# Kernel tuning notes

Hardware: AMD Instinct MI355X
Metric: run time of the kernel (lower is better)

## Reference

```python
import jax, jax.numpy as jnp
import numpy as np

B, H, S, D = 2, 12, 4096, 64

def setup_inputs() -> dict:
    key = jax.random.key(0)
    kq, kk, kv = jax.random.split(key, 3)
    Q = jax.random.normal(kq, (B, H, S, D), dtype=jnp.float32)
    K = jax.random.normal(kk, (B, H, S, D), dtype=jnp.float32)
    V = jax.random.normal(kv, (B, H, S, D), dtype=jnp.float32)
    attn_mask = jnp.zeros((1, 1, 1, 1), dtype=bool)  # unused by the original forward
    return {"Q": Q, "K": K, "V": V, "attn_mask": attn_mask}

def reference(Q, K, V, attn_mask):
    d_k = K.shape[3]
    # scores: [B, H, S, S] -- naive full materialization, matching the original
    scores = jnp.einsum("bhqd,bhkd->bhqk", Q, K) / np.sqrt(d_k).astype(Q.dtype)
    attn = jax.nn.softmax(scores, axis=-1)
    context = jnp.einsum("bhqk,bhkd->bhqd", attn, V)
    return context
```

## Files before the change

### kernel.cpp

```cpp
#include <hip/hip_runtime.h>

typedef _Float16 half4_t __attribute__((ext_vector_type(4)));
typedef _Float16 half8_t __attribute__((ext_vector_type(8)));
typedef __fp16  fp16x2_t __attribute__((ext_vector_type(2)));
typedef float floatx4 __attribute__((ext_vector_type(4)));

constexpr int S_  = 4096;
constexpr int D_  = 64;
constexpr int NBH = 24;
constexpr int BM  = 128;
constexpr int BN  = 64;
constexpr float SC2 = 0.125f * 1.44269504088896340736f;

__global__ __launch_bounds__(256) void preconv(
    const float* __restrict__ K, const float* __restrict__ V,
    _Float16* __restrict__ Kh, _Float16* __restrict__ Vh)
{
  __shared__ float tile[64 * 68];
  const int kt = blockIdx.x, bh = blockIdx.y, tid = threadIdx.x;
  const size_t tbase = ((size_t)bh * 64 + kt) * 4096;
#pragma unroll
  for (int it = 0; it < 2; ++it) {
    size_t i = tbase + (size_t)(tid + 256 * it) * 8;
    float4 a = *(const float4*)(K + i);
    float4 b = *(const float4*)(K + i + 4);
    *(half8_t*)(Kh + i) = (half8_t){
      (_Float16)(a.x*SC2),(_Float16)(a.y*SC2),(_Float16)(a.z*SC2),(_Float16)(a.w*SC2),
      (_Float16)(b.x*SC2),(_Float16)(b.y*SC2),(_Float16)(b.z*SC2),(_Float16)(b.w*SC2) };
  }
#pragma unroll
  for (int it = 0; it < 4; ++it) {
    int r  = (tid >> 4) + 16 * it;
    int c4 = (tid & 15) * 4;
    *(float4*)(&tile[r * 68 + c4]) = *(const float4*)(V + tbase + (size_t)r * 64 + c4);
  }
  __syncthreads();
  const int d = tid >> 2;
  _Float16 out[16];
#pragma unroll
  for (int j = 0; j < 16; ++j) {
    int key = 32 * (j >> 3) + 16 * ((j >> 2) & 1) + 4 * (tid & 3) + (j & 3);
    out[j] = (_Float16)tile[key * 68 + d];
  }
  _Float16* dst = Vh + tbase + (size_t)d * 64 + (tid & 3) * 16;
  *(half8_t*)(dst)     = *(half8_t*)(&out[0]);
  *(half8_t*)(dst + 8) = *(half8_t*)(&out[8]);
}


__device__ __forceinline__ void async16(const _Float16* g, _Float16* l) {
  __builtin_amdgcn_global_load_lds((const __attribute__((address_space(1))) void*)g,
                                   (__attribute__((address_space(3))) void*)l, 16, 0, 0);
}

__global__ __launch_bounds__(512, 4) void fattn2(
    const float* __restrict__ Qf, const _Float16* __restrict__ Kh,
    const _Float16* __restrict__ Vh, float* __restrict__ O)
{
  __shared__ __align__(16) _Float16 smem[6 * 4096];

  const int tid  = threadIdx.x;
  const int lane = tid & 63;
  const int w    = tid >> 6;
  const int g    = lane >> 4;
  const int m    = lane & 15;
  const int qh   = w & 3;
  const int kh2  = w >> 2;

  const int bid  = blockIdx.x;
  const int xcd  = bid & 7;
  const int slot = bid >> 3;
  const int bh   = xcd * 3 + (slot >> 5);
  const int qblk = slot & 31;
  const size_t base = (size_t)bh * S_ * D_;
  const int q0g = qblk * BM + qh * 32;

  half8_t qf[2][2];
#pragma unroll
  for (int qt = 0; qt < 2; ++qt)
#pragma unroll
    for (int ks = 0; ks < 2; ++ks) {
      const float4* qp = (const float4*)(Qf + base + (size_t)(q0g + qt*16 + m) * D_ + 8*g + 32*ks);
      float4 a = qp[0], b = qp[1];
      qf[qt][ks] = (half8_t){ (_Float16)a.x,(_Float16)a.y,(_Float16)a.z,(_Float16)a.w,
                              (_Float16)b.x,(_Float16)b.y,(_Float16)b.z,(_Float16)b.w };
    }

  floatx4 oacc[2][4];
#pragma unroll
  for (int qt = 0; qt < 2; ++qt)
#pragma unroll
    for (int db = 0; db < 4; ++db) oacc[qt][db] = (floatx4){0.f,0.f,0.f,0.f};
  float lsum[2] = {0.f, 0.f};

  const int goff0 = (tid >> 3) * 64 + (((tid & 7) ^ ((tid >> 3) & 7)) << 3);
  const int l0 = w * 512;

  const _Float16* Kb = Kh + base;
  const _Float16* Vb = Vh + base;

  _Float16 *k0 = smem,          *k1 = smem + 4096,  *k2 = smem + 8192;
  _Float16 *v0 = smem + 12288,  *v1 = smem + 16384, *v2 = smem + 20480;

  auto stage = [&](_Float16* kd, _Float16* vd, int kt) {
    const _Float16* Kt = Kb + ((size_t)kt << 12);
    const _Float16* Vt = Vb + ((size_t)kt << 12);
    async16(Kt + goff0, kd + l0);
    async16(Vt + goff0, vd + l0);
  };

  stage(k0, v0, 0);
  stage(k1, v1, 1);

  const int r7 = m & 7;
  const int krow = 32 * kh2 + m;

  for (int kt = 0; kt < 64; ++kt) {
    asm volatile("s_waitcnt vmcnt(2)\n\ts_barrier" ::: "memory");
    stage(k2, v2, (kt + 2) & 63);

    half8_t kf[2][2];
#pragma unroll
    for (int nb2 = 0; nb2 < 2; ++nb2) {
      kf[nb2][0] = *(const half8_t*)(&k0[(krow + 16*nb2) * 64 + ((g    ) ^ r7) * 8]);
      kf[nb2][1] = *(const half8_t*)(&k0[(krow + 16*nb2) * 64 + ((g + 4) ^ r7) * 8]);
    }
    half8_t vf[4];
#pragma unroll
    for (int db = 0; db < 4; ++db)
      vf[db] = *(const half8_t*)(&v0[(16*db + m) * 64 + ((2*g + kh2) ^ r7) * 8]);

#pragma unroll
    for (int qt = 0; qt < 2; ++qt) {
      floatx4 s0 = (floatx4){0.f,0.f,0.f,0.f};
      floatx4 s1 = (floatx4){0.f,0.f,0.f,0.f};
      s0 = __builtin_amdgcn_mfma_f32_16x16x32_f16(kf[0][0], qf[qt][0], s0, 0, 0, 0);
      s0 = __builtin_amdgcn_mfma_f32_16x16x32_f16(kf[0][1], qf[qt][1], s0, 0, 0, 0);
      s1 = __builtin_amdgcn_mfma_f32_16x16x32_f16(kf[1][0], qf[qt][0], s1, 0, 0, 0);
      s1 = __builtin_amdgcn_mfma_f32_16x16x32_f16(kf[1][1], qf[qt][1], s1, 0, 0, 0);

      float p0 = __builtin_amdgcn_exp2f(s0[0]);
      float p1 = __builtin_amdgcn_exp2f(s0[1]);
      float p2 = __builtin_amdgcn_exp2f(s0[2]);
      float p3 = __builtin_amdgcn_exp2f(s0[3]);
      float p4 = __builtin_amdgcn_exp2f(s1[0]);
      float p5 = __builtin_amdgcn_exp2f(s1[1]);
      float p6 = __builtin_amdgcn_exp2f(s1[2]);
      float p7 = __builtin_amdgcn_exp2f(s1[3]);
      lsum[qt] += (p0 + p1 + p2 + p3) + (p4 + p5 + p6 + p7);

      union { half8_t h8; fp16x2_t h2[4]; } pu;
      pu.h2[0] = __builtin_amdgcn_cvt_pkrtz(p0, p1);
      pu.h2[1] = __builtin_amdgcn_cvt_pkrtz(p2, p3);
      pu.h2[2] = __builtin_amdgcn_cvt_pkrtz(p4, p5);
      pu.h2[3] = __builtin_amdgcn_cvt_pkrtz(p6, p7);

#pragma unroll
      for (int db = 0; db < 4; ++db)
        oacc[qt][db] = __builtin_amdgcn_mfma_f32_16x16x32_f16(pu.h8, vf[db], oacc[qt][db], 0, 0, 0);
    }

    _Float16* t;
    t = k0; k0 = k1; k1 = k2; k2 = t;
    t = v0; v0 = v1; v1 = v2; v2 = t;
  }

  __syncthreads();
  float* red  = (float*)smem;
  float* lred = red + 10240;
  const int ro = qh * 2560;

  if (kh2 == 1) {
#pragma unroll
    for (int qt = 0; qt < 2; ++qt) {
#pragma unroll
      for (int db = 0; db < 4; ++db)
        *(floatx4*)(&red[ro + (16*db + m) * 40 + qt*16 + 4*g]) = oacc[qt][db];
      float l = lsum[qt];
      l += __shfl_xor(l, 16);
      l += __shfl_xor(l, 32);
      lred[qh * 32 + qt*16 + m] = l;
    }
  }
  __syncthreads();
  if (kh2 == 0) {
#pragma unroll
    for (int qt = 0; qt < 2; ++qt) {
      float l = lsum[qt];
      l += __shfl_xor(l, 16);
      l += __shfl_xor(l, 32);
      l += lred[qh * 32 + qt*16 + m];
      floatx4 linv;
#pragma unroll
      for (int r = 0; r < 4; ++r)
        linv[r] = 1.0f / __shfl(l, (lane & 48) + 4*g + r);
      float* Op = O + base + (size_t)(q0g + qt*16) * D_;
#pragma unroll
      for (int db = 0; db < 4; ++db) {
        floatx4 part = *(const floatx4*)(&red[ro + (16*db + m) * 40 + qt*16 + 4*g]);
        floatx4 o = oacc[qt][db] + part;
#pragma unroll
        for (int r = 0; r < 4; ++r)
          Op[(size_t)(4*g + r) * D_ + 16*db + m] = o[r] * linv[r];
      }
    }
  }
}

constexpr int SKf = 72;
constexpr int SVf = 68;
__global__ __launch_bounds__(256, 3) void fattn_fb(
    const float* __restrict__ Q, const float* __restrict__ K,
    const float* __restrict__ V, float* __restrict__ O)
{
  __shared__ __align__(16) _Float16 Ks[2][64 * SKf];
  __shared__ __align__(16) _Float16 Vs[2][64 * SVf];
  const int tid = threadIdx.x, lane = tid & 63, w = tid >> 6, g = lane >> 4, m = lane & 15;
  const int bid = blockIdx.x, xcd = bid & 7, slot = bid >> 3;
  const int bh = xcd * 3 + (slot >> 5), qblk = slot & 31;
  const size_t base = (size_t)bh * S_ * D_;
  const int q0 = qblk * BM + w * 32;
  half8_t qf[2][2];
#pragma unroll
  for (int qt = 0; qt < 2; ++qt)
#pragma unroll
    for (int ks = 0; ks < 2; ++ks) {
      const float4* qp = (const float4*)(Q + base + (size_t)(q0 + qt*16 + m) * D_ + 8*g + 32*ks);
      float4 a = qp[0], b = qp[1];
      qf[qt][ks] = (half8_t){ (_Float16)(a.x*SC2),(_Float16)(a.y*SC2),(_Float16)(a.z*SC2),(_Float16)(a.w*SC2),
                              (_Float16)(b.x*SC2),(_Float16)(b.y*SC2),(_Float16)(b.z*SC2),(_Float16)(b.w*SC2) };
    }
  floatx4 oacc[2][4];
#pragma unroll
  for (int qt = 0; qt < 2; ++qt)
#pragma unroll
    for (int db = 0; db < 4; ++db) oacc[qt][db] = (floatx4){0.f,0.f,0.f,0.f};
  float lsum[2] = {0.f, 0.f};
  const float* Kb = K + base; const float* Vb = V + base;
  float4 kreg[4]; float vreg[16];
  const int sL = ((lane >> 2) ^ (lane >> 4)) & 3;
  auto issue = [&](int kt) {
    const float* Kt = Kb + (size_t)kt * BN * D_;
#pragma unroll
    for (int it = 0; it < 2; ++it) {
      int sl = tid + 256*it; int key = sl >> 3; int c8 = (sl & 7) << 3;
      const float4* p = (const float4*)(Kt + (size_t)key * D_ + c8);
      kreg[2*it] = p[0]; kreg[2*it+1] = p[1];
    }
    const float* Vt = Vb + (size_t)kt * BN * D_;
#pragma unroll
    for (int it = 0; it < 4; ++it) {
      int kb = it * 16 + (w << 2);
      const float* vp = Vt + (size_t)kb * D_ + lane;
      vreg[4*it+0]=vp[0]; vreg[4*it+1]=vp[D_]; vreg[4*it+2]=vp[2*D_]; vreg[4*it+3]=vp[3*D_];
    }
  };
  auto commit = [&](int buf) {
    _Float16* Kd = Ks[buf]; _Float16* Vd = Vs[buf];
#pragma unroll
    for (int it = 0; it < 2; ++it) {
      int sl = tid + 256*it; int key = sl >> 3; int c8 = (sl & 7) << 3;
      float4 a = kreg[2*it], b = kreg[2*it+1];
      *(half8_t*)(&Kd[key * SKf + c8]) = (half8_t){ (_Float16)a.x,(_Float16)a.y,(_Float16)a.z,(_Float16)a.w,
                                                    (_Float16)b.x,(_Float16)b.y,(_Float16)b.z,(_Float16)b.w };
    }
#pragma unroll
    for (int it = 0; it < 4; ++it)
      *(half4_t*)(&Vd[lane * SVf + 4 * ((4*it + w) ^ sL)]) =
        (half4_t){ (_Float16)vreg[4*it+0], (_Float16)vreg[4*it+1], (_Float16)vreg[4*it+2], (_Float16)vreg[4*it+3] };
  };
  issue(0); commit(0); __syncthreads();
  const int s0i = m >> 2;
  for (int kt = 0; kt < 64; ++kt) {
    const int cur = kt & 1;
    if (kt < 63) issue(kt + 1);
    const _Float16* Kd = Ks[cur]; const _Float16* Vd = Vs[cur];
    half8_t kf[4][2];
#pragma unroll
    for (int nb = 0; nb < 4; ++nb) {
      kf[nb][0] = *(const half8_t*)(&Kd[(16*nb + m) * SKf + 8*g]);
      kf[nb][1] = *(const half8_t*)(&Kd[(16*nb + m) * SKf + 8*g + 32]);
    }
    half4_t vf[4][4];
#pragma unroll
    for (int nb = 0; nb < 4; ++nb)
#pragma unroll
      for (int db = 0; db < 4; ++db)
        vf[nb][db] = *(const half4_t*)(&Vd[(16*db + m) * SVf + 4 * ((4*nb + g) ^ s0i ^ db)]);
#pragma unroll
    for (int qt = 0; qt < 2; ++qt) {
      floatx4 sacc[4];
#pragma unroll
      for (int nb = 0; nb < 4; ++nb) {
        floatx4 acc = (floatx4){0.f,0.f,0.f,0.f};
        acc = __builtin_amdgcn_mfma_f32_16x16x32_f16(kf[nb][0], qf[qt][0], acc, 0, 0, 0);
        acc = __builtin_amdgcn_mfma_f32_16x16x32_f16(kf[nb][1], qf[qt][1], acc, 0, 0, 0);
        sacc[nb] = acc;
      }
      half4_t pf[4]; float ls = 0.f;
#pragma unroll
      for (int nb = 0; nb < 4; ++nb) {
        float p0 = __builtin_amdgcn_exp2f(sacc[nb][0]); float p1 = __builtin_amdgcn_exp2f(sacc[nb][1]);
        float p2 = __builtin_amdgcn_exp2f(sacc[nb][2]); float p3 = __builtin_amdgcn_exp2f(sacc[nb][3]);
        ls += p0 + p1 + p2 + p3;
        pf[nb] = (half4_t){ (_Float16)p0, (_Float16)p1, (_Float16)p2, (_Float16)p3 };
      }
      lsum[qt] += ls;
#pragma unroll
      for (int nb = 0; nb < 4; ++nb)
#pragma unroll
        for (int db = 0; db < 4; ++db)
          oacc[qt][db] = __builtin_amdgcn_mfma_f32_16x16x16f16(pf[nb], vf[nb][db], oacc[qt][db], 0, 0, 0);
    }
    if (kt < 63) commit(1 - cur);
    __syncthreads();
  }
#pragma unroll
  for (int qt = 0; qt < 2; ++qt) {
    float l = lsum[qt];
    l += __shfl_xor(l, 16); l += __shfl_xor(l, 32);
    floatx4 linv;
#pragma unroll
    for (int r = 0; r < 4; ++r) linv[r] = 1.0f / __shfl(l, (lane & 48) + 4*g + r);
    float* Op = O + base + (size_t)(q0 + qt*16) * D_;
#pragma unroll
    for (int db = 0; db < 4; ++db)
#pragma unroll
      for (int r = 0; r < 4; ++r)
        Op[(size_t)(4*g + r) * D_ + 16*db + m] = oacc[qt][db][r] * linv[r];
  }
}

extern "C" void kernel_launch(void* const* d_in, const int* in_sizes, int n_in,
                              void* d_out, int out_size, void* d_ws, size_t ws_size,
                              hipStream_t stream) {
  const float* Q = (const float*)d_in[0];
  const float* K = (const float*)d_in[1];
  const float* V = (const float*)d_in[2];
  float* Out = (float*)d_out;

  constexpr size_t NELEM = (size_t)NBH * S_ * D_;
  constexpr size_t NEED  = 2 * NELEM * sizeof(_Float16);

  if (ws_size >= NEED) {
    _Float16* Khp = (_Float16*)d_ws;
    _Float16* Vhp = Khp + NELEM;
    preconv<<<dim3(64, NBH), 256, 0, stream>>>(K, V, Khp, Vhp);
    fattn2<<<NBH * (S_ / BM), 512, 0, stream>>>(Q, Khp, Vhp, Out);
  } else {
    fattn_fb<<<NBH * (S_ / BM), 256, 0, stream>>>(Q, K, V, Out);
  }
}
```

Before: 210.0 us.

## Switch K/V LDS pipeline to double-buffered pairs of tiles per barrier

Replaces the three-stage rotating K/V LDS ring with two read and two write buffers. Each loop iteration waits for all loads, issues two tiles of prefetch and computes two tiles, so there is one barrier per two key tiles. The aim is to halve barrier and waitcnt synchronisation overhead. In exchange LDS use grows from 48KB to 64KB per block, which may reduce occupancy, and the wait is now vmcnt(0) instead of a partial wait.

```diff
diff --git a/kernel.cpp b/kernel.cpp
--- a/kernel.cpp
+++ b/kernel.cpp
@@ -57,7 +57,7 @@
     const float* __restrict__ Qf, const _Float16* __restrict__ Kh,
     const _Float16* __restrict__ Vh, float* __restrict__ O)
 {
-  __shared__ __align__(16) _Float16 smem[6 * 4096];
+  __shared__ __align__(16) _Float16 smem[8 * 4096];
 
   const int tid  = threadIdx.x;
   const int lane = tid & 63;
@@ -99,8 +99,10 @@
   const _Float16* Kb = Kh + base;
   const _Float16* Vb = Vh + base;
 
-  _Float16 *k0 = smem,          *k1 = smem + 4096,  *k2 = smem + 8192;
-  _Float16 *v0 = smem + 12288,  *v1 = smem + 16384, *v2 = smem + 20480;
+  _Float16 *kr0 = smem,           *kr1 = smem + 4096;
+  _Float16 *kw0 = smem + 8192,    *kw1 = smem + 12288;
+  _Float16 *vr0 = smem + 16384,   *vr1 = smem + 20480;
+  _Float16 *vw0 = smem + 24576,   *vw1 = smem + 28672;
 
   auto stage = [&](_Float16* kd, _Float16* vd, int kt) {
     const _Float16* Kt = Kb + ((size_t)kt << 12);
@@ -109,26 +111,20 @@
     async16(Vt + goff0, vd + l0);
   };
 
-  stage(k0, v0, 0);
-  stage(k1, v1, 1);
-
   const int r7 = m & 7;
   const int krow = 32 * kh2 + m;
 
-  for (int kt = 0; kt < 64; ++kt) {
-    asm volatile("s_waitcnt vmcnt(2)\n\ts_barrier" ::: "memory");
-    stage(k2, v2, (kt + 2) & 63);
-
+  auto compute = [&](const _Float16* kbuf, const _Float16* vbuf) {
     half8_t kf[2][2];
 #pragma unroll
     for (int nb2 = 0; nb2 < 2; ++nb2) {
-      kf[nb2][0] = *(const half8_t*)(&k0[(krow + 16*nb2) * 64 + ((g    ) ^ r7) * 8]);
-      kf[nb2][1] = *(const half8_t*)(&k0[(krow + 16*nb2) * 64 + ((g + 4) ^ r7) * 8]);
+      kf[nb2][0] = *(const half8_t*)(&kbuf[(krow + 16*nb2) * 64 + ((g    ) ^ r7) * 8]);
+      kf[nb2][1] = *(const half8_t*)(&kbuf[(krow + 16*nb2) * 64 + ((g + 4) ^ r7) * 8]);
     }
     half8_t vf[4];
 #pragma unroll
     for (int db = 0; db < 4; ++db)
-      vf[db] = *(const half8_t*)(&v0[(16*db + m) * 64 + ((2*g + kh2) ^ r7) * 8]);
+      vf[db] = *(const half8_t*)(&vbuf[(16*db + m) * 64 + ((2*g + kh2) ^ r7) * 8]);
 
 #pragma unroll
     for (int qt = 0; qt < 2; ++qt) {
@@ -159,10 +155,24 @@
       for (int db = 0; db < 4; ++db)
         oacc[qt][db] = __builtin_amdgcn_mfma_f32_16x16x32_f16(pu.h8, vf[db], oacc[qt][db], 0, 0, 0);
     }
+  };
+
+  stage(kr0, vr0, 0);
+  stage(kr1, vr1, 1);
+
+  for (int it = 0; it < 32; ++it) {
+    asm volatile("s_waitcnt vmcnt(0)\n\ts_barrier" ::: "memory");
+    stage(kw0, vw0, (2*it + 2) & 63);
+    stage(kw1, vw1, (2*it + 3) & 63);
+
+    compute(kr0, vr0);
+    compute(kr1, vr1);
 
     _Float16* t;
-    t = k0; k0 = k1; k1 = k2; k2 = t;
-    t = v0; v0 = v1; v1 = v2; v2 = t;
+    t = kr0; kr0 = kw0; kw0 = t;
+    t = kr1; kr1 = kw1; kw1 = t;
+    t = vr0; vr0 = vw0; vw0 = t;
+    t = vr1; vr1 = vw1; vw1 = t;
   }
 
   __syncthreads();
```

Result: no change. 209.9 us (-0.0%).
